# Kernel optimization log

Hardware: AMD Instinct MI355X
Metric: run time of the kernel (lower is better)

The kernel has to match this reference:

```python
import jax, jax.numpy as jnp
import numpy as np

EPS = 1e-6

def gram_schmidt_orthonormalize(U, eps=EPS):
    # U: [B, K, D] -> orthonormalized along K, vectorized over batch
    B, K, D = U.shape
    vs = []
    for i in range(K):
        v = U[:, i]  # [B, D]
        for vj in vs:
            coeff = jnp.sum(v * vj, axis=1, keepdims=True) / (jnp.sum(vj * vj, axis=1, keepdims=True) + eps)
            v = v - coeff * vj
        norm = jnp.maximum(jnp.linalg.norm(v, axis=1, keepdims=True), eps)
        vs.append(v / norm)
    return jnp.stack(vs, axis=1)  # [B, K, D]

def setup_inputs() -> dict:
    key = jax.random.key(0)
    ks = jax.random.split(key, 14)
    B, IN, H1, H2, OUT, E, G = 4096, 1024, 2048, 2048, 512, 8, 256
    s = 0.02
    return {
        "x":   jax.random.normal(ks[0], (B, IN), jnp.float32),
        "W1":  jax.random.normal(ks[1], (E, IN, H1), jnp.float32) * s,
        "b1":  jnp.zeros((E, H1), jnp.float32),
        "W2":  jax.random.normal(ks[2], (E, H1, H2), jnp.float32) * s,
        "b2":  jnp.zeros((E, H2), jnp.float32),
        "W3":  jax.random.normal(ks[3], (E, H2, OUT), jnp.float32) * s,
        "b3":  jnp.zeros((E, OUT), jnp.float32),
        "Wg1": jax.random.normal(ks[4], (IN, G), jnp.float32) * s,
        "bg1": jnp.zeros((G,), jnp.float32),
        "Wg2": jax.random.normal(ks[5], (G, E), jnp.float32) * s,
        "bg2": jnp.zeros((E,), jnp.float32),
        "Wo":  jax.random.normal(ks[6], (OUT, 1), jnp.float32) * s,
        "bo":  jnp.zeros((1,), jnp.float32),
    }

def reference(x, W1, b1, W2, b2, W3, b3, Wg1, bg1, Wg2, bg2, Wo, bo):
    # Expert MLPs, batched over expert axis e: [B,E,h]
    h = jax.nn.relu(jnp.einsum('bi,eih->beh', x, W1) + b1)
    h = jax.nn.relu(jnp.einsum('beh,ehk->bek', h, W2) + b2)
    expert_outputs = jnp.einsum('bek,ekd->bed', h, W3) + b3  # [B, E, D]
    # Gating network: MLP + softmax over experts
    g = jax.nn.relu(x @ Wg1 + bg1)
    gate_weights = jax.nn.softmax(g @ Wg2 + bg2, axis=-1)  # [B, E]
    # Per-sample Gram-Schmidt across experts, weighted combine
    ortho = gram_schmidt_orthonormalize(expert_outputs)  # [B, E, D]
    combined = jnp.einsum('bed,be->bd', ortho, gate_weights)  # [B, D]
    final = combined @ Wo + bo  # [B, 1]
    return (final, 0.0)
```

## Files before the change

kernel.cpp:

```cpp
#include <hip/hip_runtime.h>
#include <hip/hip_bf16.h>

#define DEVINL __device__ __forceinline__

constexpr int Bsz = 4096, INF = 1024, H1 = 2048, H2 = 2048, OUTD = 512, NE = 8, G = 256;

typedef __attribute__((ext_vector_type(8))) short bf16x8;
typedef __attribute__((ext_vector_type(4))) float f32x4;
typedef unsigned short u16;

DEVINL u16 f2bf(float f) {
  unsigned int u = __float_as_uint(f);
  u = (u + 0x7FFFu + ((u >> 16) & 1u)) >> 16;
  return (u16)u;
}
DEVINL float bf2f(u16 h) { return __uint_as_float((unsigned int)h << 16); }

DEVINL void gload16(const void* g, void* l) {
  __builtin_amdgcn_global_load_lds(
      (const __attribute__((address_space(1))) void*)g,
      (__attribute__((address_space(3))) void*)l, 16, 0, 0);
}

DEVINL float waveAllSum(float v) {
#pragma unroll
  for (int m = 32; m > 0; m >>= 1) v += __shfl_xor(v, m, 64);
  return v;
}

__global__ __launch_bounds__(256) void pack_wt(const float* __restrict__ W,
                                               u16* __restrict__ Th,
                                               u16* __restrict__ Tl,
                                               int K, int N) {
  __shared__ float t[32][33];
  const int e = blockIdx.z;
  W += (size_t)e * K * N;
  Th += (size_t)e * N * K;
  Tl += (size_t)e * N * K;
  const int n0 = blockIdx.x * 32, k0 = blockIdx.y * 32;
  const int r = threadIdx.x >> 3, c = (threadIdx.x & 7) * 4;
  float4 v = *(const float4*)&W[(size_t)(k0 + r) * N + n0 + c];
  t[r][c + 0] = v.x; t[r][c + 1] = v.y; t[r][c + 2] = v.z; t[r][c + 3] = v.w;
  __syncthreads();
  float o0 = t[c + 0][r], o1 = t[c + 1][r], o2 = t[c + 2][r], o3 = t[c + 3][r];
  short4 h, l;
  h.x = f2bf(o0); l.x = f2bf(o0 - bf2f(h.x));
  h.y = f2bf(o1); l.y = f2bf(o1 - bf2f(h.y));
  h.z = f2bf(o2); l.z = f2bf(o2 - bf2f(h.z));
  h.w = f2bf(o3); l.w = f2bf(o3 - bf2f(h.w));
  *(short4*)&Th[(size_t)(n0 + r) * K + k0 + c] = h;
  *(short4*)&Tl[(size_t)(n0 + r) * K + k0 + c] = l;
}

__global__ __launch_bounds__(512, 2) void gemm_2bar(
    const u16* __restrict__ Ahi, const u16* __restrict__ Alo,
    const u16* __restrict__ Bhi, const u16* __restrict__ Blo,
    const float* __restrict__ bias,
    u16* __restrict__ Chi, u16* __restrict__ Clo,
    int M, int N, int K, size_t strideAe) {
  const int e = blockIdx.x;
  Ahi += (size_t)e * strideAe;
  Alo += (size_t)e * strideAe;
  Bhi += (size_t)e * (size_t)N * K;
  Blo += (size_t)e * (size_t)N * K;
  bias += (size_t)e * N;
  Chi += (size_t)e * (size_t)M * N;
  Clo += (size_t)e * (size_t)M * N;

  const int bm = blockIdx.y * 256, bn = blockIdx.z * 256;
  __shared__ __align__(16) char ldsb[163840];
  const int lane = threadIdx.x & 63, wid = threadIdx.x >> 6;
  const int wm = wid >> 2, wn = wid & 3;
  const int l15 = lane & 15, l4 = lane >> 4;
  const int bhalf = wn >> 1, jn = wn & 1;

  f32x4 acc[8][4];
#pragma unroll
  for (int i = 0; i < 8; ++i)
#pragma unroll
    for (int j = 0; j < 4; ++j) acc[i][j] = (f32x4){0.f, 0.f, 0.f, 0.f};

  const int nt = K / 32;

  auto stageA = [&](const u16* src, int T, int slot, int ldsOp) {
#pragma unroll
    for (int q = 0; q < 2; ++q) {
      const int g = wid * 2 + q;
      gload16(src + (size_t)(bm + g * 16 + l15) * K + T * 32 + l4 * 8,
              ldsb + ldsOp + slot * 16384 + g * 1024);
    }
  };
  auto stageB = [&](int T, int h) {
    const int s = T & 1;
#pragma unroll
    for (int q = 0; q < 2; ++q) {
      const int g = wid * 2 + q;
      const u16* src = (g < 8) ? Bhi : Blo;
      const int f = g & 7;
      gload16(src + (size_t)(bn + h * 128 + f * 16 + l15) * K + T * 32 + l4 * 8,
              ldsb + ((g < 8) ? 98304 : 131072) + s * 16384 + h * 8192 + f * 1024);
    }
  };

  bf16x8 ah[4], al[4], bh[4], bl[4];
  auto readA = [&](int slot, int ih) {
#pragma unroll
    for (int i = 0; i < 4; ++i) {
      const int off = slot * 16384 + wm * 8192 + (ih * 4 + i) * 1024 + lane * 16;
      ah[i] = *(const bf16x8*)(ldsb + off);
      al[i] = *(const bf16x8*)(ldsb + 49152 + off);
    }
  };
  auto readBall = [&](int sB) {
#pragma unroll
    for (int j = 0; j < 4; ++j) {
      const int off = sB * 16384 + bhalf * 8192 + (jn * 4 + j) * 1024 + lane * 16;
      bh[j] = *(const bf16x8*)(ldsb + 98304 + off);
      bl[j] = *(const bf16x8*)(ldsb + 131072 + off);
    }
  };

#define QUAD48(IH)                                                             \
  _Pragma("unroll") for (int i = 0; i < 4; ++i) {                              \
    _Pragma("unroll") for (int j = 0; j < 4; ++j) {                            \
      f32x4 a = acc[(IH)*4 + i][j];                                            \
      a = __builtin_amdgcn_mfma_f32_16x16x32_bf16(bh[j], ah[i], a, 0, 0, 0);   \
      a = __builtin_amdgcn_mfma_f32_16x16x32_bf16(bl[j], ah[i], a, 0, 0, 0);   \
      a = __builtin_amdgcn_mfma_f32_16x16x32_bf16(bh[j], al[i], a, 0, 0, 0);   \
      acc[(IH)*4 + i][j] = a;                                                  \
    }                                                                          \
  }

  stageB(0, 0); stageB(0, 1);
  stageA(Ahi, 0, 0, 0); stageA(Alo, 0, 0, 49152);
  stageB(1, 0); stageB(1, 1);
  stageA(Ahi, 1, 1, 0); stageA(Alo, 1, 1, 49152);
  asm volatile("s_waitcnt vmcnt(8)" ::: "memory");
  __builtin_amdgcn_sched_barrier(0);
  __builtin_amdgcn_s_barrier();
  __builtin_amdgcn_sched_barrier(0);

  int aS = 0, aS2 = 2;
  for (int t = 0; t < nt - 2; ++t) {
    const int sB = t & 1;
    readA(aS, 0);
    readBall(sB);
    __builtin_amdgcn_sched_barrier(0);
    stageA(Ahi, t + 2, aS2, 0); stageA(Alo, t + 2, aS2, 49152);
    QUAD48(0);
    __builtin_amdgcn_sched_barrier(0);
    __builtin_amdgcn_s_barrier();
    __builtin_amdgcn_sched_barrier(0);
    readA(aS, 1);
    __builtin_amdgcn_sched_barrier(0);
    stageB(t + 2, 0); stageB(t + 2, 1);
    QUAD48(1);
    asm volatile("s_waitcnt vmcnt(8)" ::: "memory");
    __builtin_amdgcn_sched_barrier(0);
    __builtin_amdgcn_s_barrier();
    __builtin_amdgcn_sched_barrier(0);
    aS = (aS == 2) ? 0 : aS + 1;
    aS2 = (aS2 == 2) ? 0 : aS2 + 1;
  }
  {
    const int sB = (nt - 2) & 1;
    readA(aS, 0);
    readBall(sB);
    QUAD48(0);
    readA(aS, 1);
    QUAD48(1);
    asm volatile("s_waitcnt vmcnt(0)" ::: "memory");
    __builtin_amdgcn_sched_barrier(0);
    __builtin_amdgcn_s_barrier();
    __builtin_amdgcn_sched_barrier(0);
    aS = (aS == 2) ? 0 : aS + 1;
  }
  {
    const int sB = (nt - 1) & 1;
    readA(aS, 0);
    readBall(sB);
    QUAD48(0);
    readA(aS, 1);
    QUAD48(1);
  }
#undef QUAD48

#pragma unroll
  for (int i = 0; i < 8; ++i) {
    const int grow = bm + wm * 128 + i * 16 + l15;
#pragma unroll
    for (int j = 0; j < 4; ++j) {
      const int gcol = bn + wn * 64 + j * 16 + l4 * 4;
      const float4 bb = *(const float4*)&bias[gcol];
      float v0 = fmaxf(acc[i][j][0] + bb.x, 0.f);
      float v1 = fmaxf(acc[i][j][1] + bb.y, 0.f);
      float v2 = fmaxf(acc[i][j][2] + bb.z, 0.f);
      float v3 = fmaxf(acc[i][j][3] + bb.w, 0.f);
      short4 h, l;
      h.x = f2bf(v0); l.x = f2bf(v0 - bf2f(h.x));
      h.y = f2bf(v1); l.y = f2bf(v1 - bf2f(h.y));
      h.z = f2bf(v2); l.z = f2bf(v2 - bf2f(h.z));
      h.w = f2bf(v3); l.w = f2bf(v3 - bf2f(h.w));
      *(short4*)&Chi[(size_t)grow * N + gcol] = h;
      *(short4*)&Clo[(size_t)grow * N + gcol] = l;
    }
  }
}

__global__ __launch_bounds__(512, 2) void gemm_l3(
    const u16* __restrict__ Ahi, const u16* __restrict__ Alo,
    const u16* __restrict__ Bhi, const u16* __restrict__ Blo,
    const float* __restrict__ bias, float* __restrict__ Cf,
    int M, int N, int K, size_t strideAe) {
  const int e = blockIdx.x;
  Ahi += (size_t)e * strideAe;
  Alo += (size_t)e * strideAe;
  Bhi += (size_t)e * (size_t)N * K;
  Blo += (size_t)e * (size_t)N * K;
  bias += (size_t)e * N;
  Cf += (size_t)e * (size_t)M * N;

  const int bm = blockIdx.y * 128, bn = blockIdx.z * 256;
  __shared__ __align__(16) char ldsb[114688];
  const int lane = threadIdx.x & 63, wid = threadIdx.x >> 6;
  const int wm = wid >> 2, wn = wid & 3;
  const int l15 = lane & 15, l4 = lane >> 4;
  const int bhalf = wn >> 1, jn = wn & 1;

  f32x4 acc[4][4];
#pragma unroll
  for (int i = 0; i < 4; ++i)
#pragma unroll
    for (int j = 0; j < 4; ++j) acc[i][j] = (f32x4){0.f, 0.f, 0.f, 0.f};

  const int nt = K / 32;

  auto stageA3 = [&](int T, int slot) {
#pragma unroll
    for (int q = 0; q < 2; ++q) {
      const int g = wid * 2 + q;
      const u16* src = (g < 8) ? Ahi : Alo;
      const int f = g & 7;
      gload16(src + (size_t)(bm + f * 16 + l15) * K + T * 32 + l4 * 8,
              ldsb + ((g < 8) ? 0 : 24576) + slot * 8192 + f * 1024);
    }
  };
  auto stageB = [&](int T, int h) {
    const int s = T & 1;
#pragma unroll
    for (int q = 0; q < 2; ++q) {
      const int g = wid * 2 + q;
      const u16* src = (g < 8) ? Bhi : Blo;
      const int f = g & 7;
      gload16(src + (size_t)(bn + h * 128 + f * 16 + l15) * K + T * 32 + l4 * 8,
              ldsb + ((g < 8) ? 49152 : 81920) + s * 16384 + h * 8192 + f * 1024);
    }
  };

  bf16x8 ah[2], al[2], bh[4], bl[4];
  auto readA = [&](int slot, int ih) {
#pragma unroll
    for (int i = 0; i < 2; ++i) {
      const int off = slot * 8192 + (wm * 4 + ih * 2 + i) * 1024 + lane * 16;
      ah[i] = *(const bf16x8*)(ldsb + off);
      al[i] = *(const bf16x8*)(ldsb + 24576 + off);
    }
  };
  auto readBall = [&](int sB) {
#pragma unroll
    for (int j = 0; j < 4; ++j) {
      const int off = sB * 16384 + bhalf * 8192 + (jn * 4 + j) * 1024 + lane * 16;
      bh[j] = *(const bf16x8*)(ldsb + 49152 + off);
      bl[j] = *(const bf16x8*)(ldsb + 81920 + off);
    }
  };

#define QUAD24(IH)                                                             \
  _Pragma("unroll") for (int i = 0; i < 2; ++i) {                              \
    _Pragma("unroll") for (int j = 0; j < 4; ++j) {                            \
      f32x4 a = acc[(IH)*2 + i][j];                                            \
      a = __builtin_amdgcn_mfma_f32_16x16x32_bf16(bh[j], ah[i], a, 0, 0, 0);   \
      a = __builtin_amdgcn_mfma_f32_16x16x32_bf16(bl[j], ah[i], a, 0, 0, 0);   \
      a = __builtin_amdgcn_mfma_f32_16x16x32_bf16(bh[j], al[i], a, 0, 0, 0);   \
      acc[(IH)*2 + i][j] = a;                                                  \
    }                                                                          \
  }

  stageB(0, 0); stageB(0, 1);
  stageA3(0, 0);
  stageB(1, 0); stageB(1, 1);
  stageA3(1, 1);
  asm volatile("s_waitcnt vmcnt(6)" ::: "memory");
  __builtin_amdgcn_sched_barrier(0);
  __builtin_amdgcn_s_barrier();
  __builtin_amdgcn_sched_barrier(0);

  int aS = 0, aS2 = 2;
  for (int t = 0; t < nt - 2; ++t) {
    const int sB = t & 1;
    readA(aS, 0);
    readBall(sB);
    __builtin_amdgcn_sched_barrier(0);
    stageA3(t + 2, aS2);
    QUAD24(0);
    __builtin_amdgcn_sched_barrier(0);
    __builtin_amdgcn_s_barrier();
    __builtin_amdgcn_sched_barrier(0);
    readA(aS, 1);
    __builtin_amdgcn_sched_barrier(0);
    stageB(t + 2, 0); stageB(t + 2, 1);
    QUAD24(1);
    asm volatile("s_waitcnt vmcnt(6)" ::: "memory");
    __builtin_amdgcn_sched_barrier(0);
    __builtin_amdgcn_s_barrier();
    __builtin_amdgcn_sched_barrier(0);
    aS = (aS == 2) ? 0 : aS + 1;
    aS2 = (aS2 == 2) ? 0 : aS2 + 1;
  }
  {
    const int sB = (nt - 2) & 1;
    readA(aS, 0);
    readBall(sB);
    QUAD24(0);
    readA(aS, 1);
    QUAD24(1);
    asm volatile("s_waitcnt vmcnt(0)" ::: "memory");
    __builtin_amdgcn_sched_barrier(0);
    __builtin_amdgcn_s_barrier();
    __builtin_amdgcn_sched_barrier(0);
    aS = (aS == 2) ? 0 : aS + 1;
  }
  {
    const int sB = (nt - 1) & 1;
    readA(aS, 0);
    readBall(sB);
    QUAD24(0);
    readA(aS, 1);
    QUAD24(1);
  }
#undef QUAD24

#pragma unroll
  for (int i = 0; i < 4; ++i) {
    const int grow = bm + wm * 64 + i * 16 + l15;
#pragma unroll
    for (int j = 0; j < 4; ++j) {
      const int gcol = bn + wn * 64 + j * 16 + l4 * 4;
      const float4 bb = *(const float4*)&bias[gcol];
      *(float4*)&Cf[(size_t)grow * N + gcol] =
          make_float4(acc[i][j][0] + bb.x, acc[i][j][1] + bb.y,
                      acc[i][j][2] + bb.z, acc[i][j][3] + bb.w);
    }
  }
}

__global__ __launch_bounds__(256) void gate1_kernel(
    const float* __restrict__ x, const float* __restrict__ Wg1,
    const float* __restrict__ bg1, float* __restrict__ g,
    u16* __restrict__ xhi, u16* __restrict__ xlo) {
  __shared__ float xs[8 * 1024];
  const int b0 = blockIdx.x * 8;
  const size_t base = (size_t)b0 * INF;
  const float* xp = x + base;
  for (int idx = threadIdx.x * 4; idx < 8 * 1024; idx += 1024) {
    float4 v = *(const float4*)&xp[idx];
    *(float4*)&xs[idx] = v;
    short4 h, l;
    h.x = f2bf(v.x); l.x = f2bf(v.x - bf2f(h.x));
    h.y = f2bf(v.y); l.y = f2bf(v.y - bf2f(h.y));
    h.z = f2bf(v.z); l.z = f2bf(v.z - bf2f(h.z));
    h.w = f2bf(v.w); l.w = f2bf(v.w - bf2f(h.w));
    *(short4*)&xhi[base + idx] = h;
    *(short4*)&xlo[base + idx] = l;
  }
  __syncthreads();
  const int t = threadIdx.x;
  float acc[8] = {0, 0, 0, 0, 0, 0, 0, 0};
  for (int i = 0; i < INF; ++i) {
    float w = Wg1[(size_t)i * G + t];
#pragma unroll
    for (int r = 0; r < 8; ++r) acc[r] = fmaf(xs[r * 1024 + i], w, acc[r]);
  }
  const float bb = bg1[t];
#pragma unroll
  for (int r = 0; r < 8; ++r)
    g[(size_t)(b0 + r) * G + t] = fmaxf(acc[r] + bb, 0.0f);
}

__global__ __launch_bounds__(64) void gate2_kernel(
    const float* __restrict__ g, const float* __restrict__ Wg2,
    const float* __restrict__ bg2, float* __restrict__ gw) {
  const int b = blockIdx.x, lane = threadIdx.x;
  float4 gv = *(const float4*)(g + (size_t)b * G + lane * 4);
  float p[8];
#pragma unroll
  for (int e = 0; e < 8; ++e) {
    int j = lane * 4;
    float s = gv.x * Wg2[(j + 0) * 8 + e] + gv.y * Wg2[(j + 1) * 8 + e] +
              gv.z * Wg2[(j + 2) * 8 + e] + gv.w * Wg2[(j + 3) * 8 + e];
    p[e] = waveAllSum(s);
  }
  if (lane == 0) {
    float l[8];
    float mx = -1e30f;
#pragma unroll
    for (int e = 0; e < 8; ++e) {
      l[e] = p[e] + bg2[e];
      mx = fmaxf(mx, l[e]);
    }
    float sum = 0.0f;
#pragma unroll
    for (int e = 0; e < 8; ++e) {
      l[e] = expf(l[e] - mx);
      sum += l[e];
    }
    float inv = 1.0f / sum;
#pragma unroll
    for (int e = 0; e < 8; ++e) gw[(size_t)b * 8 + e] = l[e] * inv;
  }
}

__global__ __launch_bounds__(256) void gs_kernel(
    const float* __restrict__ eo, const float* __restrict__ gw,
    const float* __restrict__ Wo, const float* __restrict__ bo,
    float* __restrict__ out, int CB) {
  const int lane = threadIdx.x & 63;
  const int b = blockIdx.x * 4 + (threadIdx.x >> 6);
  const size_t ES = (size_t)CB * OUTD;
  const float* base = eo + (size_t)b * OUTD + lane * 8;
  float vs[8][8];
  float denom[8];
#pragma unroll
  for (int i = 0; i < 8; ++i) {
    float cur[8];
    float4 u0 = *(const float4*)(base + (size_t)i * ES);
    float4 u1 = *(const float4*)(base + (size_t)i * ES + 4);
    cur[0] = u0.x; cur[1] = u0.y; cur[2] = u0.z; cur[3] = u0.w;
    cur[4] = u1.x; cur[5] = u1.y; cur[6] = u1.z; cur[7] = u1.w;
#pragma unroll
    for (int j = 0; j < i; ++j) {
      float dp = 0.0f;
#pragma unroll
      for (int d = 0; d < 8; ++d) dp = fmaf(cur[d], vs[j][d], dp);
      dp = waveAllSum(dp);
      float coeff = dp / (denom[j] + 1e-6f);
#pragma unroll
      for (int d = 0; d < 8; ++d) cur[d] = fmaf(-coeff, vs[j][d], cur[d]);
    }
    float nn = 0.0f;
#pragma unroll
    for (int d = 0; d < 8; ++d) nn = fmaf(cur[d], cur[d], nn);
    nn = waveAllSum(nn);
    float inv = 1.0f / fmaxf(sqrtf(nn), 1e-6f);
#pragma unroll
    for (int d = 0; d < 8; ++d) vs[i][d] = cur[d] * inv;
    float dd = 0.0f;
#pragma unroll
    for (int d = 0; d < 8; ++d) dd = fmaf(vs[i][d], vs[i][d], dd);
    denom[i] = waveAllSum(dd);
  }
  float gwv[8];
#pragma unroll
  for (int e = 0; e < 8; ++e) gwv[e] = gw[(size_t)b * 8 + e];
  float part = 0.0f;
#pragma unroll
  for (int d = 0; d < 8; ++d) {
    float c = 0.0f;
#pragma unroll
    for (int e = 0; e < 8; ++e) c = fmaf(vs[e][d], gwv[e], c);
    part = fmaf(c, Wo[lane * 8 + d], part);
  }
  part = waveAllSum(part);
  if (lane == 0) out[b] = part + bo[0];
}

extern "C" void kernel_launch(void* const* d_in, const int* in_sizes, int n_in,
                              void* d_out, int out_size, void* d_ws, size_t ws_size,
                              hipStream_t stream) {
  const float* x   = (const float*)d_in[0];
  const float* W1  = (const float*)d_in[1];
  const float* b1  = (const float*)d_in[2];
  const float* W2  = (const float*)d_in[3];
  const float* b2  = (const float*)d_in[4];
  const float* W3  = (const float*)d_in[5];
  const float* b3  = (const float*)d_in[6];
  const float* Wg1 = (const float*)d_in[7];
  const float* bg1 = (const float*)d_in[8];
  const float* Wg2 = (const float*)d_in[9];
  const float* bg2 = (const float*)d_in[10];
  const float* Wo  = (const float*)d_in[11];
  const float* bo  = (const float*)d_in[12];
  float* out = (float*)d_out;

  char* p = (char*)d_ws;
  float* gw = (float*)p;          p += (size_t)(128u << 10);
  float* g  = (float*)p;          p += (size_t)(4u << 20);
  u16* xhi = (u16*)p;             p += (size_t)Bsz * INF * 2;
  u16* xlo = (u16*)p;             p += (size_t)Bsz * INF * 2;
  u16* w1h = (u16*)p;             p += (size_t)NE * H1 * INF * 2;
  u16* w1l = (u16*)p;             p += (size_t)NE * H1 * INF * 2;
  u16* w2h = (u16*)p;             p += (size_t)NE * H2 * H1 * 2;
  u16* w2l = (u16*)p;             p += (size_t)NE * H2 * H1 * 2;
  u16* w3h = (u16*)p;             p += (size_t)NE * OUTD * H2 * 2;
  u16* w3l = (u16*)p;             p += (size_t)NE * OUTD * H2 * 2;
  const size_t fixedBytes = (size_t)(p - (char*)d_ws);

  int CB = 4096;
  while (CB > 256 && fixedBytes + (size_t)CB * (size_t)(128u << 10) > ws_size) CB >>= 1;
  u16* h1h = (u16*)p;
  u16* h1l = h1h + (size_t)NE * CB * H1;
  u16* h2h = h1l + (size_t)NE * CB * H1;
  u16* h2l = h2h + (size_t)NE * CB * H2;
  float* eo = (float*)h1h;

  hipMemsetAsync(d_out, 0, (size_t)out_size * sizeof(float), stream);

  gate1_kernel<<<Bsz / 8, 256, 0, stream>>>(x, Wg1, bg1, g, xhi, xlo);
  gate2_kernel<<<Bsz, 64, 0, stream>>>(g, Wg2, bg2, gw);

  pack_wt<<<dim3(H1 / 32, INF / 32, NE), 256, 0, stream>>>(W1, w1h, w1l, INF, H1);
  pack_wt<<<dim3(H2 / 32, H1 / 32, NE), 256, 0, stream>>>(W2, w2h, w2l, H1, H2);
  pack_wt<<<dim3(OUTD / 32, H2 / 32, NE), 256, 0, stream>>>(W3, w3h, w3l, H2, OUTD);

  for (int c0 = 0; c0 < Bsz; c0 += CB) {
    gemm_2bar<<<dim3(NE, CB / 256, H1 / 256), 512, 0, stream>>>(
        xhi + (size_t)c0 * INF, xlo + (size_t)c0 * INF, w1h, w1l, b1,
        h1h, h1l, CB, H1, INF, (size_t)0);
    gemm_2bar<<<dim3(NE, CB / 256, H2 / 256), 512, 0, stream>>>(
        h1h, h1l, w2h, w2l, b2, h2h, h2l, CB, H2, H1, (size_t)CB * H1);
    gemm_l3<<<dim3(NE, CB / 128, OUTD / 256), 512, 0, stream>>>(
        h2h, h2l, w3h, w3l, b3, eo, CB, OUTD, H2, (size_t)CB * H2);
    gs_kernel<<<CB / 4, 256, 0, stream>>>(eo, gw + (size_t)c0 * NE, Wo, bo,
                                          out + c0, CB);
  }
}
```

Baseline: 1.523 ms.

## Swap pipeline buffering: triple-buffer B, double-buffer A, one barrier per k-step

Both expert GEMM kernels change their LDS software pipeline. B tiles now get three buffers loaded two steps ahead, and A tiles get two buffers loaded one step ahead. The mid-iteration barrier is gone, leaving one barrier per k-tile. The aim is to cut synchronisation stalls and give the larger B stream more prefetch distance, at the cost of a shorter lookahead for A and changed LDS sizing.

```diff
diff --git a/kernel.cpp b/kernel.cpp
--- a/kernel.cpp
+++ b/kernel.cpp
@@ -82,7 +82,8 @@
 
   const int nt = K / 32;
 
-  auto stageA = [&](const u16* src, int T, int slot, int ldsOp) {
+  auto stageA = [&](const u16* src, int T, int ldsOp) {
+    const int slot = T & 1;
 #pragma unroll
     for (int q = 0; q < 2; ++q) {
       const int g = wid * 2 + q;
@@ -90,15 +91,14 @@
               ldsb + ldsOp + slot * 16384 + g * 1024);
     }
   };
-  auto stageB = [&](int T, int h) {
-    const int s = T & 1;
-#pragma unroll
-    for (int q = 0; q < 2; ++q) {
-      const int g = wid * 2 + q;
-      const u16* src = (g < 8) ? Bhi : Blo;
-      const int f = g & 7;
-      gload16(src + (size_t)(bn + h * 128 + f * 16 + l15) * K + T * 32 + l4 * 8,
-              ldsb + ((g < 8) ? 98304 : 131072) + s * 16384 + h * 8192 + f * 1024);
+  auto stageB = [&](int T, int slot) {
+#pragma unroll
+    for (int q = 0; q < 4; ++q) {
+      const int g = wid * 4 + q;
+      const u16* src = (g < 16) ? Bhi : Blo;
+      const int f = g & 15;
+      gload16(src + (size_t)(bn + f * 16 + l15) * K + T * 32 + l4 * 8,
+              ldsb + ((g < 16) ? 65536 : 114688) + slot * 16384 + f * 1024);
     }
   };
 
@@ -108,15 +108,15 @@
     for (int i = 0; i < 4; ++i) {
       const int off = slot * 16384 + wm * 8192 + (ih * 4 + i) * 1024 + lane * 16;
       ah[i] = *(const bf16x8*)(ldsb + off);
-      al[i] = *(const bf16x8*)(ldsb + 49152 + off);
+      al[i] = *(const bf16x8*)(ldsb + 32768 + off);
     }
   };
   auto readBall = [&](int sB) {
 #pragma unroll
     for (int j = 0; j < 4; ++j) {
       const int off = sB * 16384 + bhalf * 8192 + (jn * 4 + j) * 1024 + lane * 16;
-      bh[j] = *(const bf16x8*)(ldsb + 98304 + off);
-      bl[j] = *(const bf16x8*)(ldsb + 131072 + off);
+      bh[j] = *(const bf16x8*)(ldsb + 65536 + off);
+      bl[j] = *(const bf16x8*)(ldsb + 114688 + off);
     }
   };
 
@@ -131,56 +131,53 @@
     }                                                                          \
   }
 
-  stageB(0, 0); stageB(0, 1);
-  stageA(Ahi, 0, 0, 0); stageA(Alo, 0, 0, 49152);
-  stageB(1, 0); stageB(1, 1);
-  stageA(Ahi, 1, 1, 0); stageA(Alo, 1, 1, 49152);
-  asm volatile("s_waitcnt vmcnt(8)" ::: "memory");
+  stageB(0, 0);
+  stageA(Ahi, 0, 0); stageA(Alo, 0, 32768);
+  stageB(1, 1);
+  asm volatile("s_waitcnt vmcnt(4)" ::: "memory");
   __builtin_amdgcn_sched_barrier(0);
   __builtin_amdgcn_s_barrier();
   __builtin_amdgcn_sched_barrier(0);
 
-  int aS = 0, aS2 = 2;
+  int bS = 0, bS2 = 2;
   for (int t = 0; t < nt - 2; ++t) {
-    const int sB = t & 1;
-    readA(aS, 0);
-    readBall(sB);
-    __builtin_amdgcn_sched_barrier(0);
-    stageA(Ahi, t + 2, aS2, 0); stageA(Alo, t + 2, aS2, 49152);
+    const int sA = t & 1;
+    readA(sA, 0);
+    readBall(bS);
+    __builtin_amdgcn_sched_barrier(0);
+    stageA(Ahi, t + 1, 0); stageA(Alo, t + 1, 32768);
+    stageB(t + 2, bS2);
     QUAD48(0);
+    readA(sA, 1);
+    QUAD48(1);
+    asm volatile("s_waitcnt vmcnt(4)" ::: "memory");
     __builtin_amdgcn_sched_barrier(0);
     __builtin_amdgcn_s_barrier();
     __builtin_amdgcn_sched_barrier(0);
-    readA(aS, 1);
-    __builtin_amdgcn_sched_barrier(0);
-    stageB(t + 2, 0); stageB(t + 2, 1);
-    QUAD48(1);
-    asm volatile("s_waitcnt vmcnt(8)" ::: "memory");
-    __builtin_amdgcn_sched_barrier(0);
-    __builtin_amdgcn_s_barrier();
-    __builtin_amdgcn_sched_barrier(0);
-    aS = (aS == 2) ? 0 : aS + 1;
-    aS2 = (aS2 == 2) ? 0 : aS2 + 1;
+    bS = (bS == 2) ? 0 : bS + 1;
+    bS2 = (bS2 == 2) ? 0 : bS2 + 1;
   }
   {
-    const int sB = (nt - 2) & 1;
-    readA(aS, 0);
-    readBall(sB);
+    const int sA = (nt - 2) & 1;
+    readA(sA, 0);
+    readBall(bS);
+    __builtin_amdgcn_sched_barrier(0);
+    stageA(Ahi, nt - 1, 0); stageA(Alo, nt - 1, 32768);
     QUAD48(0);
-    readA(aS, 1);
+    readA(sA, 1);
     QUAD48(1);
     asm volatile("s_waitcnt vmcnt(0)" ::: "memory");
     __builtin_amdgcn_sched_barrier(0);
     __builtin_amdgcn_s_barrier();
     __builtin_amdgcn_sched_barrier(0);
-    aS = (aS == 2) ? 0 : aS + 1;
+    bS = (bS == 2) ? 0 : bS + 1;
   }
   {
-    const int sB = (nt - 1) & 1;
-    readA(aS, 0);
-    readBall(sB);
+    const int sA = (nt - 1) & 1;
+    readA(sA, 0);
+    readBall(bS);
     QUAD48(0);
-    readA(aS, 1);
+    readA(sA, 1);
     QUAD48(1);
   }
 #undef QUAD48
@@ -221,7 +218,7 @@
   Cf += (size_t)e * (size_t)M * N;
 
   const int bm = blockIdx.y * 128, bn = blockIdx.z * 256;
-  __shared__ __align__(16) char ldsb[114688];
+  __shared__ __align__(16) char ldsb[131072];
   const int lane = threadIdx.x & 63, wid = threadIdx.x >> 6;
   const int wm = wid >> 2, wn = wid & 3;
   const int l15 = lane & 15, l4 = lane >> 4;
@@ -235,25 +232,25 @@
 
   const int nt = K / 32;
 
-  auto stageA3 = [&](int T, int slot) {
+  auto stageA3 = [&](int T) {
+    const int slot = T & 1;
 #pragma unroll
     for (int q = 0; q < 2; ++q) {
       const int g = wid * 2 + q;
       const u16* src = (g < 8) ? Ahi : Alo;
       const int f = g & 7;
       gload16(src + (size_t)(bm + f * 16 + l15) * K + T * 32 + l4 * 8,
-              ldsb + ((g < 8) ? 0 : 24576) + slot * 8192 + f * 1024);
-    }
-  };
-  auto stageB = [&](int T, int h) {
-    const int s = T & 1;
-#pragma unroll
-    for (int q = 0; q < 2; ++q) {
-      const int g = wid * 2 + q;
-      const u16* src = (g < 8) ? Bhi : Blo;
-      const int f = g & 7;
-      gload16(src + (size_t)(bn + h * 128 + f * 16 + l15) * K + T * 32 + l4 * 8,
-              ldsb + ((g < 8) ? 49152 : 81920) + s * 16384 + h * 8192 + f * 1024);
+              ldsb + ((g < 8) ? 0 : 16384) + slot * 8192 + f * 1024);
+    }
+  };
+  auto stageB = [&](int T, int slot) {
+#pragma unroll
+    for (int q = 0; q < 4; ++q) {
+      const int g = wid * 4 + q;
+      const u16* src = (g < 16) ? Bhi : Blo;
+      const int f = g & 15;
+      gload16(src + (size_t)(bn + f * 16 + l15) * K + T * 32 + l4 * 8,
+              ldsb + ((g < 16) ? 32768 : 81920) + slot * 16384 + f * 1024);
     }
   };
 
@@ -263,14 +260,14 @@
     for (int i = 0; i < 2; ++i) {
       const int off = slot * 8192 + (wm * 4 + ih * 2 + i) * 1024 + lane * 16;
       ah[i] = *(const bf16x8*)(ldsb + off);
-      al[i] = *(const bf16x8*)(ldsb + 24576 + off);
+      al[i] = *(const bf16x8*)(ldsb + 16384 + off);
     }
   };
   auto readBall = [&](int sB) {
 #pragma unroll
     for (int j = 0; j < 4; ++j) {
       const int off = sB * 16384 + bhalf * 8192 + (jn * 4 + j) * 1024 + lane * 16;
-      bh[j] = *(const bf16x8*)(ldsb + 49152 + off);
+      bh[j] = *(const bf16x8*)(ldsb + 32768 + off);
       bl[j] = *(const bf16x8*)(ldsb + 81920 + off);
     }
   };
@@ -286,56 +283,53 @@
     }                                                                          \
   }
 
-  stageB(0, 0); stageB(0, 1);
-  stageA3(0, 0);
-  stageB(1, 0); stageB(1, 1);
-  stageA3(1, 1);
-  asm volatile("s_waitcnt vmcnt(6)" ::: "memory");
+  stageB(0, 0);
+  stageA3(0);
+  stageB(1, 1);
+  asm volatile("s_waitcnt vmcnt(4)" ::: "memory");
   __builtin_amdgcn_sched_barrier(0);
   __builtin_amdgcn_s_barrier();
   __builtin_amdgcn_sched_barrier(0);
 
-  int aS = 0, aS2 = 2;
+  int bS = 0, bS2 = 2;
   for (int t = 0; t < nt - 2; ++t) {
-    const int sB = t & 1;
-    readA(aS, 0);
-    readBall(sB);
-    __builtin_amdgcn_sched_barrier(0);
-    stageA3(t + 2, aS2);
+    const int sA = t & 1;
+    readA(sA, 0);
+    readBall(bS);
+    __builtin_amdgcn_sched_barrier(0);
+    stageA3(t + 1);
+    stageB(t + 2, bS2);
     QUAD24(0);
+    readA(sA, 1);
+    QUAD24(1);
+    asm volatile("s_waitcnt vmcnt(4)" ::: "memory");
     __builtin_amdgcn_sched_barrier(0);
     __builtin_amdgcn_s_barrier();
     __builtin_amdgcn_sched_barrier(0);
-    readA(aS, 1);
-    __builtin_amdgcn_sched_barrier(0);
-    stageB(t + 2, 0); stageB(t + 2, 1);
-    QUAD24(1);
-    asm volatile("s_waitcnt vmcnt(6)" ::: "memory");
-    __builtin_amdgcn_sched_barrier(0);
-    __builtin_amdgcn_s_barrier();
-    __builtin_amdgcn_sched_barrier(0);
-    aS = (aS == 2) ? 0 : aS + 1;
-    aS2 = (aS2 == 2) ? 0 : aS2 + 1;
+    bS = (bS == 2) ? 0 : bS + 1;
+    bS2 = (bS2 == 2) ? 0 : bS2 + 1;
   }
   {
-    const int sB = (nt - 2) & 1;
-    readA(aS, 0);
-    readBall(sB);
+    const int sA = (nt - 2) & 1;
+    readA(sA, 0);
+    readBall(bS);
+    __builtin_amdgcn_sched_barrier(0);
+    stageA3(nt - 1);
     QUAD24(0);
-    readA(aS, 1);
+    readA(sA, 1);
     QUAD24(1);
     asm volatile("s_waitcnt vmcnt(0)" ::: "memory");
     __builtin_amdgcn_sched_barrier(0);
     __builtin_amdgcn_s_barrier();
     __builtin_amdgcn_sched_barrier(0);
-    aS = (aS == 2) ? 0 : aS + 1;
+    bS = (bS == 2) ? 0 : bS + 1;
   }
   {
-    const int sB = (nt - 1) & 1;
-    readA(aS, 0);
-    readBall(sB);
+    const int sA = (nt - 1) & 1;
+    readA(sA, 0);
+    readBall(bS);
     QUAD24(0);
-    readA(aS, 1);
+    readA(sA, 1);
     QUAD24(1);
   }
 #undef QUAD24
```

New measurement: 1.602 ms. +5.2%, slower.
